# Kernel tuning notes

Hardware: AMD Instinct MI355X
Metric: run time of the kernel (lower is better)

Reference implementation:

```python
import jax, jax.numpy as jnp
import numpy as np
import math

D_MODEL = 1024
NUM_HEADS = 16
D_K = D_MODEL // NUM_HEADS
D_FF = 4096
NUM_LAYERS = 6  # NOTE: the torch Encoder reuses the SAME EncoderLayer object, so weights are shared
LN_EPS = 1e-5


def _layernorm(x, scale, bias):
    mu = jnp.mean(x, axis=-1, keepdims=True)
    var = jnp.var(x, axis=-1, keepdims=True)
    return (x - mu) * jax.lax.rsqrt(var + LN_EPS) * scale + bias


def setup_inputs() -> dict:
    key = jax.random.key(0)
    ks = jax.random.split(key, 16)
    s = 0.02
    inp = {
        "x": jax.random.normal(ks[0], (2, 2048, D_MODEL), dtype=jnp.float32),
        "mask": jnp.ones((2, 1, 1, 2048), dtype=bool),
        "wq": jax.random.normal(ks[1], (D_MODEL, D_MODEL), jnp.float32) * s,
        "bq": jnp.zeros((D_MODEL,), jnp.float32),
        "wk": jax.random.normal(ks[2], (D_MODEL, D_MODEL), jnp.float32) * s,
        "bk": jnp.zeros((D_MODEL,), jnp.float32),
        "wv": jax.random.normal(ks[3], (D_MODEL, D_MODEL), jnp.float32) * s,
        "bv": jnp.zeros((D_MODEL,), jnp.float32),
        "wo": jax.random.normal(ks[4], (D_MODEL, D_MODEL), jnp.float32) * s,
        "bo": jnp.zeros((D_MODEL,), jnp.float32),
        "w1": jax.random.normal(ks[5], (D_MODEL, D_FF), jnp.float32) * s,
        "b1": jnp.zeros((D_FF,), jnp.float32),
        "w2": jax.random.normal(ks[6], (D_FF, D_MODEL), jnp.float32) * s,
        "b2": jnp.zeros((D_MODEL,), jnp.float32),
        "ln1_s": jnp.ones((D_MODEL,), jnp.float32),
        "ln1_b": jnp.zeros((D_MODEL,), jnp.float32),
        "ln2_s": jnp.ones((D_MODEL,), jnp.float32),
        "ln2_b": jnp.zeros((D_MODEL,), jnp.float32),
        "lnf_s": jnp.ones((D_MODEL,), jnp.float32),
        "lnf_b": jnp.zeros((D_MODEL,), jnp.float32),
    }
    return inp


def _attention(xn, mask, wq, bq, wk, bk, wv, bv, wo, bo):
    B, S, _ = xn.shape
    q = (xn @ wq + bq).reshape(B, S, NUM_HEADS, D_K).transpose(0, 2, 1, 3)
    k = (xn @ wk + bk).reshape(B, S, NUM_HEADS, D_K).transpose(0, 2, 1, 3)
    v = (xn @ wv + bv).reshape(B, S, NUM_HEADS, D_K).transpose(0, 2, 1, 3)
    scores = jnp.einsum("bhqd,bhkd->bhqk", q, k) / math.sqrt(D_K)  # [B,H,S,S]
    scores = jnp.where(mask, scores, jnp.float32(-1e9))
    attn = jax.nn.softmax(scores, axis=-1)
    out = jnp.einsum("bhqk,bhkd->bhqd", attn, v)
    out = out.transpose(0, 2, 1, 3).reshape(B, S, D_MODEL)
    return out @ wo + bo


def reference(x, mask, wq, bq, wk, bk, wv, bv, wo, bo, w1, b1, w2, b2,
              ln1_s, ln1_b, ln2_s, ln2_b, lnf_s, lnf_b):
    h = x
    for _ in range(NUM_LAYERS):  # shared weights across layers (faithful to source)
        # pre-LN self-attention sublayer with residual
        h = h + _attention(_layernorm(h, ln1_s, ln1_b), mask,
                           wq, bq, wk, bk, wv, bv, wo, bo)
        # pre-LN FFN sublayer with residual
        hn = _layernorm(h, ln2_s, ln2_b)
        h = h + (jax.nn.relu(hn @ w1 + b1) @ w2 + b2)
    return _layernorm(h, lnf_s, lnf_b)
```

## Files before the change

kernel.cpp:

```cpp
#include <hip/hip_runtime.h>
#include <stdint.h>


#define S_LEN 2048
#define NTOK 4096
#define MBYTE (1u << 20)

typedef __attribute__((ext_vector_type(8))) short bf16x8;
typedef __attribute__((ext_vector_type(4))) short bf16x4;
typedef __attribute__((ext_vector_type(4))) float f32x4;
typedef __attribute__((ext_vector_type(16))) float f32x16;
typedef __attribute__((ext_vector_type(4))) int i32x4;

#define MFMA16 __builtin_amdgcn_mfma_f32_16x16x32_bf16
#define MFMA32 __builtin_amdgcn_mfma_f32_32x32x16_bf16

#define S_BARRIER __builtin_amdgcn_s_barrier()
#define SCHED_FENCE __builtin_amdgcn_sched_barrier(0)
#define LGKM0 asm volatile("s_waitcnt lgkmcnt(0)" ::: "memory")
#define VMCNT(n) asm volatile("s_waitcnt vmcnt(" #n ")" ::: "memory")

static __device__ __forceinline__ short f2bf(float f) {
    union { float f; uint32_t u; } a; a.f = f;
    uint32_t r = a.u + 0x7FFFu + ((a.u >> 16) & 1u);
    return (short)(r >> 16);
}

static __device__ __forceinline__ void gload_lds16(const void* g, void* l) {
    __builtin_amdgcn_global_load_lds(
        (const __attribute__((address_space(1))) void*)g,
        (__attribute__((address_space(3))) void*)l, 16, 0, 0);
}

__global__ __launch_bounds__(256)
void transpose_cast(const float* __restrict__ in, short* __restrict__ out,
                    int R, int C)
{
    __shared__ float tile[64][65];
    const int t  = threadIdx.x;
    const int bc = blockIdx.x * 64;
    const int br = blockIdx.y * 64;
    const int rl = t >> 2;
    const int c0 = (t & 3) * 16;
    const float* src = in + (size_t)(br + rl) * C + bc + c0;
#pragma unroll
    for (int i = 0; i < 4; ++i) {
        f32x4 v = *(const f32x4*)(src + i * 4);
        tile[rl][c0 + i*4 + 0] = v[0];
        tile[rl][c0 + i*4 + 1] = v[1];
        tile[rl][c0 + i*4 + 2] = v[2];
        tile[rl][c0 + i*4 + 3] = v[3];
    }
    __syncthreads();
    const int cl = t >> 2;
    const int r0 = (t & 3) * 16;
    bf16x8 o0, o1;
#pragma unroll
    for (int j = 0; j < 8; ++j) o0[j] = f2bf(tile[r0 + j][cl]);
#pragma unroll
    for (int j = 0; j < 8; ++j) o1[j] = f2bf(tile[r0 + 8 + j][cl]);
    short* dst = out + (size_t)(bc + cl) * R + br + r0;
    *(bf16x8*)dst       = o0;
    *(bf16x8*)(dst + 8) = o1;
}

__global__ void concat_bias(const float* __restrict__ bq, const float* __restrict__ bk,
                            const float* __restrict__ bv, float* __restrict__ o)
{
    int i = blockIdx.x * 256 + threadIdx.x;
    o[i] = (i < 1024) ? bq[i] : (i < 2048) ? bk[i - 1024] : bv[i - 2048];
}

template<int OUT_F32>
__global__ __launch_bounds__(256)
void ln_kernel(const float* __restrict__ x, const float* __restrict__ sc,
               const float* __restrict__ bi, void* __restrict__ outp)
{
    const int row = blockIdx.x;
    const int t = threadIdx.x;
    const float* xr = x + (size_t)row * 1024;
    f32x4 v = *(const f32x4*)(xr + t * 4);
    float sum = v[0] + v[1] + v[2] + v[3];
    float sq  = v[0]*v[0] + v[1]*v[1] + v[2]*v[2] + v[3]*v[3];
#pragma unroll
    for (int m = 1; m <= 32; m <<= 1) {
        sum += __shfl_xor(sum, m);
        sq  += __shfl_xor(sq, m);
    }
    __shared__ float rs[4], rq[4];
    const int w = t >> 6;
    if ((t & 63) == 0) { rs[w] = sum; rq[w] = sq; }
    __syncthreads();
    sum = rs[0] + rs[1] + rs[2] + rs[3];
    sq  = rq[0] + rq[1] + rq[2] + rq[3];
    const float mu   = sum * (1.0f / 1024.0f);
    const float var  = sq * (1.0f / 1024.0f) - mu * mu;
    const float rstd = rsqrtf(var + 1e-5f);
    f32x4 s4 = *(const f32x4*)(sc + t * 4);
    f32x4 b4 = *(const f32x4*)(bi + t * 4);
    f32x4 o;
#pragma unroll
    for (int j = 0; j < 4; ++j) o[j] = (v[j] - mu) * rstd * s4[j] + b4[j];
    if (OUT_F32) {
        *(f32x4*)((float*)outp + (size_t)row * 1024 + t * 4) = o;
    } else {
        bf16x4 ob;
#pragma unroll
        for (int j = 0; j < 4; ++j) ob[j] = f2bf(o[j]);
        *(bf16x4*)((short*)outp + (size_t)row * 1024 + t * 4) = ob;
    }
}

template<int MODE>
__global__ __launch_bounds__(512, 2)
void gemm256(const short* __restrict__ A, const short* __restrict__ Bt,
             const float* __restrict__ bias, short* __restrict__ Cout,
             int M, int N, int K)
{
    __shared__ __align__(16) short LDSB[3][2][8192];
    const int t = threadIdx.x;
    const int w = t >> 6, l = t & 63;
    const int lr = l & 15, lk = l >> 4;
    const int wm = w >> 2, wn = w & 3;

    const int gx = gridDim.x;
    const int nwg = gx * gridDim.y;
    int id = blockIdx.y * gx + blockIdx.x;
    {
        const int q = nwg >> 3, r = nwg & 7;
        const int xcd = id & 7, idx = id >> 3;
        id = (xcd < r ? xcd * (q + 1) : r * (q + 1) + (xcd - r) * q) + idx;
    }
    const int bn = (id % gx) * 256;
    const int bm = (id / gx) * 256;

    f32x4 acc[8][4];
#pragma unroll
    for (int i = 0; i < 8; ++i)
#pragma unroll
        for (int j = 0; j < 4; ++j) acc[i][j] = (f32x4)0.0f;

    const int srow = t >> 2;
    const int c    = (t & 3) ^ ((t >> 3) & 3);
    const short* gA0 = A  + (size_t)(bm + srow) * K + c * 8;
    const short* gA1 = gA0 + (size_t)128 * K;
    const short* gB0 = Bt + (size_t)(bn + srow) * K + c * 8;
    const short* gB1 = gB0 + (size_t)128 * K;

    auto stageA = [&](int buf, int k0) {
        char* d = (char*)LDSB[buf][0];
        gload_lds16(gA0 + k0, d + t * 16);
        gload_lds16(gA1 + k0, d + 8192 + t * 16);
    };
    auto stageB = [&](int buf, int k0) {
        char* d = (char*)LDSB[buf][1];
        gload_lds16(gB0 + k0, d + t * 16);
        gload_lds16(gB1 + k0, d + 8192 + t * 16);
    };

    const int sl   = ((lk ^ ((lr >> 1) & 3)) << 4);
    const int arow = (wm * 128 + lr) * 64 + sl;
    const int brow = (wn * 64 + lr) * 64 + sl;

    const int nk = K >> 5;
    stageA(0, 0);  stageB(0, 0);
    stageA(1, 32); stageB(1, 32);
    VMCNT(4);
    S_BARRIER;
    SCHED_FENCE;

    for (int tt = 0; tt < nk; ++tt) {
        const int cb = tt % 3;
        const char* TA = (const char*)LDSB[cb][0];
        const char* TB = (const char*)LDSB[cb][1];
        bf16x8 af[4], bfr[4];
        if (tt + 2 < nk) stageA((tt + 2) % 3, (tt + 2) * 32);
#pragma unroll
        for (int jn = 0; jn < 4; ++jn)
            bfr[jn] = *(const bf16x8*)(TB + brow + jn * 1024);
#pragma unroll
        for (int i = 0; i < 4; ++i)
            af[i] = *(const bf16x8*)(TA + arow + i * 1024);
        LGKM0; SCHED_FENCE;
        __builtin_amdgcn_s_setprio(1);
#pragma unroll
        for (int i = 0; i < 4; ++i)
#pragma unroll
            for (int jn = 0; jn < 4; ++jn)
                acc[i][jn] = MFMA16(af[i], bfr[jn], acc[i][jn], 0, 0, 0);
        __builtin_amdgcn_s_setprio(0);
        if (tt + 2 < nk) stageB((tt + 2) % 3, (tt + 2) * 32);
#pragma unroll
        for (int i = 0; i < 4; ++i)
            af[i] = *(const bf16x8*)(TA + arow + (i + 4) * 1024);
        LGKM0; SCHED_FENCE;
        __builtin_amdgcn_s_setprio(1);
#pragma unroll
        for (int i = 0; i < 4; ++i)
#pragma unroll
            for (int jn = 0; jn < 4; ++jn)
                acc[i + 4][jn] = MFMA16(af[i], bfr[jn], acc[i + 4][jn], 0, 0, 0);
        __builtin_amdgcn_s_setprio(0);
        if (tt + 2 < nk)      { VMCNT(4); }
        else if (tt + 1 < nk) { VMCNT(0); }
        S_BARRIER;
        SCHED_FENCE;
    }

#pragma unroll
    for (int jn = 0; jn < 4; ++jn) {
        const int col = bn + wn * 64 + jn * 16 + lr;
        const float bv = bias[col];
        const float qscale = (MODE == 3 && col < 1024) ? 0.1803368801f : 1.0f;
#pragma unroll
        for (int i = 0; i < 8; ++i) {
            const int row0 = bm + wm * 128 + i * 16 + lk * 4;
#pragma unroll
            for (int r = 0; r < 4; ++r) {
                float v = acc[i][jn][r] + bv;
                if (MODE == 1) v = fmaxf(v, 0.0f);
                if (MODE == 3) v *= qscale;
                Cout[(size_t)(row0 + r) * N + col] = f2bf(v);
            }
        }
    }
}

template<int MODE>
__global__ __launch_bounds__(512, 4)
void gemm_bt(const short* __restrict__ A, const short* __restrict__ Bt,
             const float* __restrict__ bias, const float* __restrict__ res,
             void* __restrict__ Cout, int M, int N, int K)
{
    __shared__ __align__(16) short As[2][128 * 32];
    __shared__ __align__(16) short Bs[2][128 * 32];
    const int t = threadIdx.x;
    const int w = t >> 6, l = t & 63;
    const int lr = l & 15, lk = l >> 4;

    const int gx = gridDim.x;
    const int nwg = gx * gridDim.y;
    int id = blockIdx.y * gx + blockIdx.x;
    {
        const int q = nwg >> 3, r = nwg & 7;
        const int xcd = id & 7, idx = id >> 3;
        id = (xcd < r ? xcd * (q + 1) : r * (q + 1) + (xcd - r) * q) + idx;
    }
    const int bn = (id % gx) * 128;
    const int bm = (id / gx) * 128;
    const int wr = (w >> 1) * 32, wc = (w & 1) * 64;

    f32x4 acc[2][4];
#pragma unroll
    for (int i = 0; i < 2; ++i)
#pragma unroll
        for (int j = 0; j < 4; ++j) acc[i][j] = (f32x4)0.0f;

    const short* gA0 = A  + (size_t)(bm + (t >> 2)) * K + (t & 3) * 8;
    const short* gB0 = Bt + (size_t)(bn + (t >> 2)) * K + (t & 3) * 8;

    i32x4 q0[2], q1[2], q2[2], q3[2];

    auto LOADT = [&](i32x4 (&r)[2], int k0) {
        r[0] = *(const i32x4*)(gA0 + k0);
        r[1] = *(const i32x4*)(gB0 + k0);
    };
    auto WRITET = [&](int buf, const i32x4 (&r)[2]) {
        *(i32x4*)((char*)As[buf] + t * 16) = r[0];
        *(i32x4*)((char*)Bs[buf] + t * 16) = r[1];
    };
    auto COMPUTE = [&](int buf) {
        const short* Ab = As[buf];
        const short* Bb = Bs[buf];
        bf16x8 af[2], bfr[4];
#pragma unroll
        for (int i = 0; i < 2; ++i)
            af[i] = *(const bf16x8*)(Ab + (wr + i * 16 + lr) * 32 + lk * 8);
#pragma unroll
        for (int j = 0; j < 4; ++j)
            bfr[j] = *(const bf16x8*)(Bb + (wc + j * 16 + lr) * 32 + lk * 8);
#pragma unroll
        for (int i = 0; i < 2; ++i)
#pragma unroll
            for (int j = 0; j < 4; ++j)
                acc[i][j] = MFMA16(af[i], bfr[j], acc[i][j], 0, 0, 0);
    };

    const int nk = K >> 5;
    LOADT(q0, 0);
    LOADT(q1, 32);
    LOADT(q2, 64);
    LOADT(q3, 96);
    WRITET(0, q0);
    LGKM0;
    S_BARRIER;

    for (int s = 0; s < nk; s += 4) {
        WRITET(1, q1);
        if (s + 4 < nk) LOADT(q0, (s + 4) * 32);
        COMPUTE(0);
        LGKM0; S_BARRIER;
        WRITET(0, q2);
        if (s + 5 < nk) LOADT(q1, (s + 5) * 32);
        COMPUTE(1);
        LGKM0; S_BARRIER;
        WRITET(1, q3);
        if (s + 6 < nk) LOADT(q2, (s + 6) * 32);
        COMPUTE(0);
        LGKM0; S_BARRIER;
        if (s + 4 < nk) WRITET(0, q0);
        if (s + 7 < nk) LOADT(q3, (s + 7) * 32);
        COMPUTE(1);
        LGKM0; S_BARRIER;
    }

#pragma unroll
    for (int j = 0; j < 4; ++j) {
        const int col = bn + wc + j * 16 + lr;
        const float bv = bias[col];
#pragma unroll
        for (int i = 0; i < 2; ++i) {
            const int row0 = bm + wr + i * 16 + lk * 4;
#pragma unroll
            for (int r = 0; r < 4; ++r) {
                const int row = row0 + r;
                float v = acc[i][j][r] + bv;
                if (MODE == 1) v = fmaxf(v, 0.0f);
                if (MODE == 2) {
                    float* C = (float*)Cout;
                    C[(size_t)row * N + col] = v + res[(size_t)row * N + col];
                } else {
                    short* C = (short*)Cout;
                    C[(size_t)row * N + col] = f2bf(v);
                }
            }
        }
    }
}

__global__ __launch_bounds__(256)
void v_transpose(const short* __restrict__ qkv, short* __restrict__ vT)
{
    __shared__ short tile[64][72];
    const int bh = blockIdx.x;
    const int sblk = blockIdx.y;
    const int b = bh >> 4, h = bh & 15;
    const int t = threadIdx.x;
    const int sl = t >> 2;
    const int d0 = (t & 3) * 16;
    const short* src = qkv + (size_t)(b * S_LEN + sblk * 64 + sl) * 3072 + 2048 + h * 64 + d0;
    bf16x8 a = *(const bf16x8*)src;
    bf16x8 c = *(const bf16x8*)(src + 8);
#pragma unroll
    for (int j = 0; j < 8; ++j) { tile[sl][d0 + j] = a[j]; tile[sl][d0 + 8 + j] = c[j]; }
    __syncthreads();
    const int dl = t >> 2;
    const int s0 = (t & 3) * 16;
    bf16x8 o0, o1;
#pragma unroll
    for (int j = 0; j < 8; ++j) o0[j] = tile[s0 + j][dl];
#pragma unroll
    for (int j = 0; j < 8; ++j) o1[j] = tile[s0 + 8 + j][dl];
    short* dst = vT + (size_t)(bh * 64 + dl) * S_LEN + sblk * 64 + s0;
    *(bf16x8*)dst       = o0;
    *(bf16x8*)(dst + 8) = o1;
}

__global__ __launch_bounds__(256, 2)
void attn_fwd(const short* __restrict__ qkv, const short* __restrict__ vT,
              short* __restrict__ outp)
{
    __shared__ __align__(16) char Kt[2][8192];
    __shared__ __align__(16) char Vt[2][8192];

    const int bh = blockIdx.x;
    const int qblk = blockIdx.y;
    const int b = bh >> 4, h = bh & 15;
    const int t = threadIdx.x;
    const int w = t >> 6, l = t & 63;
    const int l31 = l & 31, lh = l >> 5;
    const int q0 = qblk * 128 + w * 32;

    const short* qp = qkv + (size_t)(b * S_LEN + q0 + l31) * 3072 + h * 64 + lh * 8;
    bf16x8 aq[4];
#pragma unroll
    for (int kh = 0; kh < 4; ++kh)
        aq[kh] = *(const bf16x8*)(qp + kh * 16);

    const int r0  = t >> 3;
    const int sc0 = (t & 7) ^ (r0 & 7);
    const short* kst = qkv + (size_t)(b * S_LEN + r0) * 3072 + 1024 + h * 64 + sc0 * 8;
    const short* vst = vT + (size_t)bh * 64 * S_LEN + (size_t)r0 * S_LEN + sc0 * 8;
    const int dst0 = w * 1024;
    const int dst1 = 4096 + w * 1024;

    int offs[4];
#pragma unroll
    for (int x = 0; x < 4; ++x)
        offs[x] = l31 * 128 + (((2 * x + lh) ^ (l31 & 7)) << 4);

    f32x16 acc0 = (f32x16)0.0f, acc1 = (f32x16)0.0f;
    float lsum = 0.0f;

    gload_lds16(kst,                Kt[0] + dst0);
    gload_lds16(kst + 32 * 3072,    Kt[0] + dst1);
    gload_lds16(vst,                Vt[0] + dst0);
    gload_lds16(vst + 32 * S_LEN,   Vt[0] + dst1);

    int cur = 0;
    for (int tt = 0; tt < 32; ++tt) {
        __syncthreads();
        if (tt + 1 < 32) {
            const short* kn = kst + (size_t)(tt + 1) * 64 * 3072;
            const short* vn = vst + (tt + 1) * 64;
            gload_lds16(kn,              Kt[cur ^ 1] + dst0);
            gload_lds16(kn + 32 * 3072,  Kt[cur ^ 1] + dst1);
            gload_lds16(vn,              Vt[cur ^ 1] + dst0);
            gload_lds16(vn + 32 * S_LEN, Vt[cur ^ 1] + dst1);
        }
        const char* K = Kt[cur];
        const char* V = Vt[cur];

#pragma unroll
        for (int jb = 0; jb < 2; ++jb) {
            f32x16 st = (f32x16)0.0f;
#pragma unroll
            for (int kh = 0; kh < 4; ++kh) {
                bf16x8 kf = *(const bf16x8*)(K + jb * 4096 + offs[kh]);
                st = MFMA32(kf, aq[kh], st, 0, 0, 0);
            }
            uint32_t wd[8];
#pragma unroll
            for (int m = 0; m < 8; ++m) {
                float pa = __builtin_amdgcn_exp2f(st[2 * m]);
                float pb = __builtin_amdgcn_exp2f(st[2 * m + 1]);
                lsum += pa + pb;
                asm("v_cvt_pk_bf16_f32 %0, %1, %2" : "=v"(wd[m]) : "v"(pa), "v"(pb));
            }
#pragma unroll
            for (int ksl = 0; ksl < 2; ++ksl) {
                uint32_t x0 = wd[4 * ksl + 2], y0 = wd[4 * ksl];
                uint32_t x1 = wd[4 * ksl + 3], y1 = wd[4 * ksl + 1];
                asm("v_permlane32_swap_b32 %0, %1" : "+v"(x0), "+v"(y0));
                asm("v_permlane32_swap_b32 %0, %1" : "+v"(x1), "+v"(y1));
                union { uint32_t u[4]; bf16x8 v; } fr;
                fr.u[0] = y0; fr.u[1] = y1; fr.u[2] = x0; fr.u[3] = x1;
                const int ks = jb * 2 + ksl;
                bf16x8 vf0 = *(const bf16x8*)(V + offs[ks]);
                bf16x8 vf1 = *(const bf16x8*)(V + 4096 + offs[ks]);
                acc0 = MFMA32(vf0, fr.v, acc0, 0, 0, 0);
                acc1 = MFMA32(vf1, fr.v, acc1, 0, 0, 0);
            }
        }
        cur ^= 1;
    }

    lsum += __shfl_xor(lsum, 32);
    const float inv = 1.0f / lsum;

    const size_t orow = (size_t)(b * S_LEN + q0 + l31) * 1024 + h * 64;
#pragma unroll
    for (int reg = 0; reg < 16; ++reg) {
        const int dl = (reg & 3) + 8 * (reg >> 2) + 4 * lh;
        outp[orow + dl]      = f2bf(acc0[reg] * inv);
        outp[orow + 32 + dl] = f2bf(acc1[reg] * inv);
    }
}

extern "C" void kernel_launch(void* const* d_in, const int* in_sizes, int n_in,
                              void* d_out, int out_size, void* d_ws, size_t ws_size,
                              hipStream_t stream)
{
    const float* x     = (const float*)d_in[0];
    const float* wq    = (const float*)d_in[2];
    const float* bq    = (const float*)d_in[3];
    const float* wk    = (const float*)d_in[4];
    const float* bk    = (const float*)d_in[5];
    const float* wv    = (const float*)d_in[6];
    const float* bv    = (const float*)d_in[7];
    const float* wo    = (const float*)d_in[8];
    const float* bo    = (const float*)d_in[9];
    const float* w1    = (const float*)d_in[10];
    const float* b1    = (const float*)d_in[11];
    const float* w2    = (const float*)d_in[12];
    const float* b2    = (const float*)d_in[13];
    const float* ln1_s = (const float*)d_in[14];
    const float* ln1_b = (const float*)d_in[15];
    const float* ln2_s = (const float*)d_in[16];
    const float* ln2_b = (const float*)d_in[17];
    const float* lnf_s = (const float*)d_in[18];
    const float* lnf_b = (const float*)d_in[19];

    char* ws = (char*)d_ws;
    if (ws_size < (size_t)89 * MBYTE) return;

    float* h     = (float*)(ws);
    short* xn    = (short*)(ws + (size_t)16 * MBYTE);
    short* qkvb  = (short*)(ws + (size_t)24 * MBYTE);
    short* vT    = (short*)(ws + (size_t)48 * MBYTE);
    short* aout  = (short*)(ws + (size_t)56 * MBYTE);
    short* ffh   = (short*)(ws + (size_t)24 * MBYTE);
    short* wqkvT = (short*)(ws + (size_t)64 * MBYTE);
    short* woT   = (short*)(ws + (size_t)70 * MBYTE);
    short* w1T   = (short*)(ws + (size_t)72 * MBYTE);
    short* w2T   = (short*)(ws + (size_t)80 * MBYTE);
    float* bqkv  = (float*)(ws + (size_t)88 * MBYTE);

    transpose_cast<<<dim3(16, 16), 256, 0, stream>>>(wq, wqkvT,               1024, 1024);
    transpose_cast<<<dim3(16, 16), 256, 0, stream>>>(wk, wqkvT + 1024 * 1024, 1024, 1024);
    transpose_cast<<<dim3(16, 16), 256, 0, stream>>>(wv, wqkvT + 2048 * 1024, 1024, 1024);
    transpose_cast<<<dim3(16, 16), 256, 0, stream>>>(wo, woT,                 1024, 1024);
    transpose_cast<<<dim3(64, 16), 256, 0, stream>>>(w1, w1T, 1024, 4096);
    transpose_cast<<<dim3(16, 64), 256, 0, stream>>>(w2, w2T, 4096, 1024);
    concat_bias<<<12, 256, 0, stream>>>(bq, bk, bv, bqkv);
    hipMemcpyAsync(h, x, (size_t)NTOK * 1024 * 4, hipMemcpyDeviceToDevice, stream);

    for (int layer = 0; layer < 6; ++layer) {
        ln_kernel<0><<<NTOK, 256, 0, stream>>>(h, ln1_s, ln1_b, xn);
        gemm256<3><<<dim3(12, 16), 512, 0, stream>>>(xn, wqkvT, bqkv, qkvb,
                                                     NTOK, 3072, 1024);
        v_transpose<<<dim3(32, 32), 256, 0, stream>>>(qkvb, vT);
        attn_fwd<<<dim3(32, 16), 256, 0, stream>>>(qkvb, vT, aout);
        gemm_bt<2><<<dim3(8, 32), 512, 0, stream>>>(aout, woT, bo, h, h,
                                                    NTOK, 1024, 1024);
        ln_kernel<0><<<NTOK, 256, 0, stream>>>(h, ln2_s, ln2_b, xn);
        gemm256<1><<<dim3(16, 16), 512, 0, stream>>>(xn, w1T, b1, ffh,
                                                     NTOK, 4096, 1024);
        gemm_bt<2><<<dim3(8, 32), 512, 0, stream>>>(ffh, w2T, b2, h, h,
                                                    NTOK, 1024, 4096);
    }
    ln_kernel<1><<<NTOK, 256, 0, stream>>>(h, lnf_s, lnf_b, d_out);
}
```

Baseline: 1.298 ms.

## Replace direct global-to-LDS triple buffering with register-staged double buffering in GEMM

```diff
diff --git a/kernel.cpp b/kernel.cpp
--- a/kernel.cpp
+++ b/kernel.cpp
@@ -18,7 +18,6 @@
 #define S_BARRIER __builtin_amdgcn_s_barrier()
 #define SCHED_FENCE __builtin_amdgcn_sched_barrier(0)
 #define LGKM0 asm volatile("s_waitcnt lgkmcnt(0)" ::: "memory")
-#define VMCNT(n) asm volatile("s_waitcnt vmcnt(" #n ")" ::: "memory")
 
 static __device__ __forceinline__ short f2bf(float f) {
     union { float f; uint32_t u; } a; a.f = f;
@@ -117,7 +116,8 @@
              const float* __restrict__ bias, short* __restrict__ Cout,
              int M, int N, int K)
 {
-    __shared__ __align__(16) short LDSB[3][2][8192];
+    __shared__ __align__(16) short As[2][256 * 32];
+    __shared__ __align__(16) short Bs[2][256 * 32];
     const int t = threadIdx.x;
     const int w = t >> 6, l = t & 63;
     const int lr = l & 15, lk = l >> 4;
@@ -141,47 +141,43 @@
         for (int j = 0; j < 4; ++j) acc[i][j] = (f32x4)0.0f;
 
     const int srow = t >> 2;
-    const int c    = (t & 3) ^ ((t >> 3) & 3);
-    const short* gA0 = A  + (size_t)(bm + srow) * K + c * 8;
+    const short* gA0 = A  + (size_t)(bm + srow) * K + (t & 3) * 8;
     const short* gA1 = gA0 + (size_t)128 * K;
-    const short* gB0 = Bt + (size_t)(bn + srow) * K + c * 8;
+    const short* gB0 = Bt + (size_t)(bn + srow) * K + (t & 3) * 8;
     const short* gB1 = gB0 + (size_t)128 * K;
-
-    auto stageA = [&](int buf, int k0) {
-        char* d = (char*)LDSB[buf][0];
-        gload_lds16(gA0 + k0, d + t * 16);
-        gload_lds16(gA1 + k0, d + 8192 + t * 16);
+    const int wof = srow * 64 + (((t & 3) ^ ((srow >> 1) & 3)) << 4);
+
+    i32x4 q0[4], q1[4];
+
+    auto LOADT = [&](i32x4 (&r)[4], int k0) {
+        r[0] = *(const i32x4*)(gA0 + k0);
+        r[1] = *(const i32x4*)(gA1 + k0);
+        r[2] = *(const i32x4*)(gB0 + k0);
+        r[3] = *(const i32x4*)(gB1 + k0);
     };
-    auto stageB = [&](int buf, int k0) {
-        char* d = (char*)LDSB[buf][1];
-        gload_lds16(gB0 + k0, d + t * 16);
-        gload_lds16(gB1 + k0, d + 8192 + t * 16);
+    auto WRITET = [&](int buf, const i32x4 (&r)[4]) {
+        char* pa = (char*)As[buf];
+        char* pb = (char*)Bs[buf];
+        *(i32x4*)(pa + wof)        = r[0];
+        *(i32x4*)(pa + wof + 8192) = r[1];
+        *(i32x4*)(pb + wof)        = r[2];
+        *(i32x4*)(pb + wof + 8192) = r[3];
     };
 
     const int sl   = ((lk ^ ((lr >> 1) & 3)) << 4);
     const int arow = (wm * 128 + lr) * 64 + sl;
     const int brow = (wn * 64 + lr) * 64 + sl;
 
-    const int nk = K >> 5;
-    stageA(0, 0);  stageB(0, 0);
-    stageA(1, 32); stageB(1, 32);
-    VMCNT(4);
-    S_BARRIER;
-    SCHED_FENCE;
-
-    for (int tt = 0; tt < nk; ++tt) {
-        const int cb = tt % 3;
-        const char* TA = (const char*)LDSB[cb][0];
-        const char* TB = (const char*)LDSB[cb][1];
+    auto COMPUTE = [&](int buf) {
+        const char* TA = (const char*)As[buf];
+        const char* TB = (const char*)Bs[buf];
         bf16x8 af[4], bfr[4];
-        if (tt + 2 < nk) stageA((tt + 2) % 3, (tt + 2) * 32);
 #pragma unroll
         for (int jn = 0; jn < 4; ++jn)
             bfr[jn] = *(const bf16x8*)(TB + brow + jn * 1024);
 #pragma unroll
         for (int i = 0; i < 4; ++i)
             af[i] = *(const bf16x8*)(TA + arow + i * 1024);
-        LGKM0; SCHED_FENCE;
         __builtin_amdgcn_s_setprio(1);
 #pragma unroll
         for (int i = 0; i < 4; ++i)
@@ -189,11 +185,9 @@
             for (int jn = 0; jn < 4; ++jn)
                 acc[i][jn] = MFMA16(af[i], bfr[jn], acc[i][jn], 0, 0, 0);
         __builtin_amdgcn_s_setprio(0);
-        if (tt + 2 < nk) stageB((tt + 2) % 3, (tt + 2) * 32);
 #pragma unroll
         for (int i = 0; i < 4; ++i)
             af[i] = *(const bf16x8*)(TA + arow + (i + 4) * 1024);
-        LGKM0; SCHED_FENCE;
         __builtin_amdgcn_s_setprio(1);
 #pragma unroll
         for (int i = 0; i < 4; ++i)
@@ -201,10 +195,24 @@
             for (int jn = 0; jn < 4; ++jn)
                 acc[i + 4][jn] = MFMA16(af[i], bfr[jn], acc[i + 4][jn], 0, 0, 0);
         __builtin_amdgcn_s_setprio(0);
-        if (tt + 2 < nk)      { VMCNT(4); }
-        else if (tt + 1 < nk) { VMCNT(0); }
-        S_BARRIER;
-        SCHED_FENCE;
+    };
+
+    const int nk = K >> 5;
+    LOADT(q0, 0);
+    LOADT(q1, 32);
+    WRITET(0, q0);
+    LGKM0;
+    S_BARRIER;
+
+    for (int s = 0; s < nk; s += 2) {
+        if (s + 2 < nk) LOADT(q0, (s + 2) * 32);
+        WRITET(1, q1);
+        COMPUTE(0);
+        LGKM0; S_BARRIER;
+        if (s + 3 < nk) LOADT(q1, (s + 3) * 32);
+        if (s + 2 < nk) WRITET(0, q0);
+        COMPUTE(1);
+        LGKM0; S_BARRIER;
     }
 
 #pragma unroll
```

New measurement: 1.327 ms. +2.2%, slower.
